# Kernel tuning notes

Hardware: AMD Instinct MI355X
Metric: run time of the kernel (lower is better)

Reference implementation:

```python
import jax, jax.numpy as jnp
import numpy as np

SM_STEPS = 10

def setup_inputs() -> dict:
    key = jax.random.key(0)
    k0, k1, k2, k3 = jax.random.split(key, 4)
    B, N, D, A = 8, 2048, 512, 128
    X = jax.random.normal(k0, (B, N, D), jnp.float32)
    adj = jax.random.uniform(k1, (B, N, N), jnp.float32)
    adj = adj / jnp.sum(adj, axis=-1, keepdims=True)  # row-stochastic for stable diffusion
    mask = jnp.ones((B, N), jnp.float32)
    W1 = jax.random.normal(k2, (A, D), jnp.float32) / np.sqrt(D).astype(np.float32)
    b1 = jnp.zeros((A,), jnp.float32)
    w2 = jax.random.normal(k3, (1, A), jnp.float32) / np.sqrt(A).astype(np.float32)
    alpha_logit = jnp.zeros((), jnp.float32)  # trainable alpha = sigmoid(0) = 0.5
    return {"X": X, "adj": adj, "mask": mask, "W1": W1, "b1": b1, "w2": w2, "alpha_logit": alpha_logit}

def _sm(f, adj, alpha, num_steps):
    # approx Sm: g <- alpha * adj @ g + (1 - alpha) * f, iterated num_steps times
    def body(g, _):
        g = alpha * jnp.einsum('bij,bjd->bid', adj, g) + (1.0 - alpha) * f
        return g, None
    g, _ = jax.lax.scan(body, f, None, length=num_steps)
    return g

def reference(X, adj, mask, W1, b1, w2, alpha_logit):
    alpha = jax.nn.sigmoid(alpha_logit)
    Xs = _sm(X, adj, alpha, SM_STEPS)                     # sm_where == 'early'
    H = jnp.einsum('bnd,ad->bna', Xs, W1) + b1            # proj1: (B,N,att_dim)
    H = jax.nn.gelu(H, approximate=False)                 # torch gelu (erf)
    f = jnp.einsum('bna,oa->bno', H, w2)                  # proj2: (B,N,1)
    m = mask[..., None]                                   # (B,N,1)
    logits = jnp.where(m > 0, f, -jnp.inf)
    s = jax.nn.softmax(logits, axis=1)                    # masked softmax over bag dim
    z = jnp.einsum('bnd,bno->bd', Xs, s)                  # bmm(X^T, s).squeeze(-1)
    return z
```

## Files before the change

### kernel.cpp

```cpp
#include <hip/hip_runtime.h>

constexpr int BB = 8;
constexpr int NN = 2048;
constexpr int DD = 512;
constexpr int AA = 128;
constexpr int SM_STEPS = 10;

typedef __attribute__((ext_vector_type(8))) short bf16x8;
typedef __attribute__((ext_vector_type(4))) float f32x4;
typedef __attribute__((ext_vector_type(8))) unsigned short u16x8;

__device__ __forceinline__ float bf2f(unsigned short u) {
  unsigned int v = ((unsigned int)u) << 16;
  union { unsigned int i; float f; } c; c.i = v; return c.f;
}
__device__ __forceinline__ unsigned short f2bf(float f) {
  union { float f; unsigned int i; } c; c.f = f;
  unsigned int v = c.i;
  unsigned int r = (v + 0x7FFFu + ((v >> 16) & 1u)) >> 16;
  return (unsigned short)r;
}

#define GLOBAL_AS __attribute__((address_space(1)))
#define LDS_AS __attribute__((address_space(3)))

__device__ __forceinline__ void async16(const void* g, void* l) {
  __builtin_amdgcn_global_load_lds((GLOBAL_AS const void*)g, (LDS_AS void*)l, 16, 0, 0);
}

__global__ __launch_bounds__(256) void convert_adj_kernel(
    const float* __restrict__ adj, unsigned short* __restrict__ adjb) {
  size_t i = (size_t)blockIdx.x * blockDim.x + threadIdx.x;
  size_t total = (size_t)BB * NN * NN / 4;
  size_t stride = (size_t)gridDim.x * blockDim.x;
  for (; i < total; i += stride) {
    float4 v = ((const float4*)adj)[i];
    ushort4 o;
    o.x = f2bf(v.x); o.y = f2bf(v.y); o.z = f2bf(v.z); o.w = f2bf(v.w);
    ((ushort4*)adjb)[i] = o;
  }
}

__global__ __launch_bounds__(256) void convert_w1_kernel(
    const float* __restrict__ W1, unsigned short* __restrict__ w1b) {
  int i = blockIdx.x * 256 + threadIdx.x;
  float4 v = ((const float4*)W1)[i];
  ushort4 o;
  o.x = f2bf(v.x); o.y = f2bf(v.y); o.z = f2bf(v.z); o.w = f2bf(v.w);
  ((ushort4*)w1b)[i] = o;
}

__global__ __launch_bounds__(256) void transpose_x_kernel(
    const float* __restrict__ X, unsigned short* __restrict__ xt) {
  __shared__ float tile[64][65];
  const int b = blockIdx.z;
  const int n0 = blockIdx.x * 64, d0 = blockIdx.y * 64;
  const int t = threadIdx.x;
  for (int i = 0; i < 16; ++i) {
    int idx = t + i * 256;
    int r = idx >> 6, c = idx & 63;
    tile[r][c] = X[(size_t)b * NN * DD + (size_t)(n0 + r) * DD + d0 + c];
  }
  __syncthreads();
  for (int i = 0; i < 16; ++i) {
    int idx = t + i * 256;
    int r = idx >> 6, c = idx & 63;
    xt[(size_t)b * DD * NN + (size_t)(d0 + r) * NN + n0 + c] = f2bf(tile[c][r]);
  }
}

__global__ __launch_bounds__(256) void transpose_xs_kernel(
    const unsigned short* __restrict__ xst, unsigned short* __restrict__ gnorm) {
  __shared__ unsigned int tile[64][65];
  const int b = blockIdx.z;
  const int n0 = blockIdx.x * 64, d0 = blockIdx.y * 64;
  const int t = threadIdx.x;
  for (int i = 0; i < 16; ++i) {
    int idx = t + i * 256;
    int r = idx >> 6, c = idx & 63;
    tile[r][c] = xst[(size_t)b * DD * NN + (size_t)(d0 + r) * NN + n0 + c];
  }
  __syncthreads();
  for (int i = 0; i < 16; ++i) {
    int idx = t + i * 256;
    int r = idx >> 6, c = idx & 63;
    gnorm[(size_t)b * NN * DD + (size_t)(n0 + r) * DD + d0 + c] =
        (unsigned short)tile[c][r];
  }
}

__global__ __launch_bounds__(512) void sm_step_kernel(
    const unsigned short* __restrict__ adjb,
    const unsigned short* __restrict__ gin,
    const unsigned short* __restrict__ xt,
    unsigned short* __restrict__ gout,
    const float* __restrict__ alogit) {
  constexpr int BK = 64;
  __shared__ alignas(16) unsigned char Abuf[3][128 * BK * 2];
  __shared__ alignas(16) unsigned char Bbuf[3][256 * BK * 2];

  const int t = threadIdx.x;
  const int b = blockIdx.z;
  const int m0 = blockIdx.y * 128;
  const int n0 = blockIdx.x * 256;

  const int lane = t & 63;
  const int wave = t >> 6;
  const int wr = wave >> 2;
  const int wc = wave & 3;
  const int ln = lane & 15, kq = lane >> 4;

  const unsigned short* gA = gin + (size_t)b * DD * NN;
  const unsigned short* gB = adjb + (size_t)b * NN * NN;
  const unsigned short* aSrc[2];
  const unsigned short* bSrc[4];
  int aOff[2], bOff[4];
#pragma unroll
  for (int u = 0; u < 2; ++u) {
    int o = u * 8192 + t * 16;
    int q = o ^ (((o >> 7) & 7) << 4);
    int row = q >> 7, colb = q & 127;
    aSrc[u] = gA + (size_t)(m0 + row) * NN + colb / 2;
    aOff[u] = o;
  }
#pragma unroll
  for (int u = 0; u < 4; ++u) {
    int o = u * 8192 + t * 16;
    int q = o ^ (((o >> 7) & 7) << 4);
    int row = q >> 7, colb = q & 127;
    bSrc[u] = gB + (size_t)(n0 + row) * NN + colb / 2;
    bOff[u] = o;
  }

  f32x4 acc[4][4];
#pragma unroll
  for (int i = 0; i < 4; ++i)
#pragma unroll
    for (int j = 0; j < 4; ++j) acc[i][j] = {0.f, 0.f, 0.f, 0.f};

  auto phase = [&](const unsigned char* Ab, const unsigned char* Bb, int ss,
                   int stg, int tnext) {
    bf16x8 av[4], bv[4];
#pragma unroll
    for (int ii = 0; ii < 4; ++ii) {
      int row = wr * 64 + ii * 16 + ln;
      int o = (row * 128 + ss * 64 + kq * 16) ^ ((row & 7) << 4);
      av[ii] = *(const bf16x8*)(Ab + o);
    }
#pragma unroll
    for (int jj = 0; jj < 4; ++jj) {
      int row = wc * 64 + jj * 16 + ln;
      int o = (row * 128 + ss * 64 + kq * 16) ^ ((row & 7) << 4);
      bv[jj] = *(const bf16x8*)(Bb + o);
    }
    if (stg == 1) {
      const int sl = tnext % 3;
      async16(aSrc[0] + tnext * BK, &Abuf[sl][aOff[0]]);
      async16(aSrc[1] + tnext * BK, &Abuf[sl][aOff[1]]);
      async16(bSrc[0] + tnext * BK, &Bbuf[sl][bOff[0]]);
    } else if (stg == 2) {
      const int sl = tnext % 3;
      async16(bSrc[1] + tnext * BK, &Bbuf[sl][bOff[1]]);
      async16(bSrc[2] + tnext * BK, &Bbuf[sl][bOff[2]]);
      async16(bSrc[3] + tnext * BK, &Bbuf[sl][bOff[3]]);
    }
    __builtin_amdgcn_s_barrier();
    asm volatile("s_waitcnt lgkmcnt(0)" ::: "memory");
    __builtin_amdgcn_sched_barrier(0);
    __builtin_amdgcn_s_setprio(1);
#pragma unroll
    for (int ii = 0; ii < 4; ++ii)
#pragma unroll
      for (int jj = 0; jj < 4; ++jj)
        acc[ii][jj] = __builtin_amdgcn_mfma_f32_16x16x32_bf16(av[ii], bv[jj],
                                                              acc[ii][jj], 0, 0, 0);
    __builtin_amdgcn_s_setprio(0);
    __builtin_amdgcn_s_barrier();
  };

#pragma unroll
  for (int tv = 0; tv < 2; ++tv) {
    const int sl = tv;
    async16(aSrc[0] + tv * BK, &Abuf[sl][aOff[0]]);
    async16(aSrc[1] + tv * BK, &Abuf[sl][aOff[1]]);
    async16(bSrc[0] + tv * BK, &Bbuf[sl][bOff[0]]);
    async16(bSrc[1] + tv * BK, &Bbuf[sl][bOff[1]]);
    async16(bSrc[2] + tv * BK, &Bbuf[sl][bOff[2]]);
    async16(bSrc[3] + tv * BK, &Bbuf[sl][bOff[3]]);
  }

  for (int tk = 0; tk < 30; ++tk) {
    const int sl = tk % 3;
    const unsigned char* Ab = Abuf[sl];
    const unsigned char* Bb = Bbuf[sl];
    asm volatile("s_waitcnt vmcnt(6)" ::: "memory");
    __builtin_amdgcn_s_barrier();
    phase(Ab, Bb, 0, 1, tk + 2);
    phase(Ab, Bb, 1, 2, tk + 2);
  }
  asm volatile("s_waitcnt vmcnt(6)" ::: "memory");
  __builtin_amdgcn_s_barrier();
  phase(Abuf[0], Bbuf[0], 0, 0, 0);
  phase(Abuf[0], Bbuf[0], 1, 0, 0);
  asm volatile("s_waitcnt vmcnt(0)" ::: "memory");
  __builtin_amdgcn_s_barrier();
  phase(Abuf[1], Bbuf[1], 0, 0, 0);
  phase(Abuf[1], Bbuf[1], 1, 0, 0);

  const float al = alogit[0];
  const float alpha = 1.0f / (1.0f + expf(-al));
  const float ia = 1.0f - alpha;

#pragma unroll
  for (int i = 0; i < 4; ++i) {
#pragma unroll
    for (int j = 0; j < 4; ++j) {
      const int mbase = m0 + wr * 64 + i * 16 + kq * 4;
      const int nn = n0 + wc * 64 + j * 16 + ln;
#pragma unroll
      for (int r = 0; r < 4; ++r) {
        size_t idx = (size_t)b * DD * NN + (size_t)(mbase + r) * NN + nn;
        float xv = bf2f(xt[idx]);
        gout[idx] = f2bf(alpha * acc[i][j][r] + ia * xv);
      }
    }
  }
}

__global__ __launch_bounds__(256) void proj_gemm_kernel(
    const unsigned short* __restrict__ gnorm,
    const unsigned short* __restrict__ w1b,
    const float* __restrict__ b1,
    const float* __restrict__ w2,
    float* __restrict__ fbuf) {
  constexpr int BK = 64;
  __shared__ alignas(16) unsigned short As[128 * BK];
  __shared__ alignas(16) unsigned short Bs[128 * BK];
  __shared__ float red[4][64];

  const int t = threadIdx.x;
  const int b = blockIdx.y;
  const int n0 = blockIdx.x * 128;

  const int lane = t & 63;
  const int wave = t >> 6;
  const int wr = wave >> 1, wc = wave & 1;
  const int ln = lane & 15, kq = lane >> 4;

  const unsigned short* gA =
      gnorm + (size_t)b * NN * DD + (size_t)(n0 + (t >> 3)) * DD + (t & 7) * 8;
  const unsigned short* gB = w1b + (size_t)(t >> 3) * DD + (t & 7) * 8;

  f32x4 acc[4][4];
#pragma unroll
  for (int i = 0; i < 4; ++i)
#pragma unroll
    for (int j = 0; j < 4; ++j) acc[i][j] = {0.f, 0.f, 0.f, 0.f};

  for (int k0 = 0; k0 < DD; k0 += BK) {
#pragma unroll
    for (int c = 0; c < 4; ++c) {
      async16(gA + (size_t)(32 * c) * DD, As + 8 * t + 2048 * c);
      async16(gB + (size_t)(32 * c) * DD, Bs + 8 * t + 2048 * c);
    }
    gA += BK;
    gB += BK;
    asm volatile("s_waitcnt vmcnt(0)" ::: "memory");
    __syncthreads();

#pragma unroll
    for (int s = 0; s < 2; ++s) {
      bf16x8 af[4], bfr[4];
#pragma unroll
      for (int i = 0; i < 4; ++i)
        af[i] = *(const bf16x8*)(&As[(wr * 64 + i * 16 + ln) * BK + s * 32 + kq * 8]);
#pragma unroll
      for (int j = 0; j < 4; ++j)
        bfr[j] = *(const bf16x8*)(&Bs[(wc * 64 + j * 16 + ln) * BK + s * 32 + kq * 8]);
#pragma unroll
      for (int i = 0; i < 4; ++i)
#pragma unroll
        for (int j = 0; j < 4; ++j)
          acc[i][j] =
              __builtin_amdgcn_mfma_f32_16x16x32_bf16(af[i], bfr[j], acc[i][j], 0, 0, 0);
    }
    __syncthreads();
  }

  float b1v[4], w2v[4];
#pragma unroll
  for (int j = 0; j < 4; ++j) {
    int a = wc * 64 + j * 16 + ln;
    b1v[j] = b1[a];
    w2v[j] = w2[a];
  }
  float p[4][4];
#pragma unroll
  for (int i = 0; i < 4; ++i)
#pragma unroll
    for (int r = 0; r < 4; ++r) {
      float s = 0.f;
#pragma unroll
      for (int j = 0; j < 4; ++j) {
        float x = acc[i][j][r] + b1v[j];
        float g = 0.5f * x * (1.0f + erff(x * 0.70710678118654752f));
        s += g * w2v[j];
      }
      p[i][r] = s;
    }
#pragma unroll
  for (int m = 1; m < 16; m <<= 1)
#pragma unroll
    for (int i = 0; i < 4; ++i)
#pragma unroll
      for (int r = 0; r < 4; ++r) p[i][r] += __shfl_xor(p[i][r], m);

  if (ln == 0) {
#pragma unroll
    for (int i = 0; i < 4; ++i)
#pragma unroll
      for (int r = 0; r < 4; ++r) red[wave][i * 16 + kq * 4 + r] = p[i][r];
  }
  __syncthreads();
  if (t < 128) {
    int w0 = (t >> 6) * 2, loc = t & 63;
    fbuf[(size_t)b * NN + n0 + t] = red[w0][loc] + red[w0 + 1][loc];
  }
}

__global__ __launch_bounds__(256) void softmax_kernel(
    const float* __restrict__ fbuf, const float* __restrict__ mask,
    float* __restrict__ sbuf) {
  __shared__ float red[8];
  const int b = blockIdx.x, t = threadIdx.x;
  float v[8];
  float mx = -INFINITY;
  for (int i = 0; i < 8; ++i) {
    int n = t + i * 256;
    float mk = mask[(size_t)b * NN + n];
    float lv = fbuf[(size_t)b * NN + n];
    v[i] = (mk > 0.f) ? lv : -INFINITY;
    mx = fmaxf(mx, v[i]);
  }
  for (int d = 32; d; d >>= 1) mx = fmaxf(mx, __shfl_xor(mx, d));
  if ((t & 63) == 0) red[t >> 6] = mx;
  __syncthreads();
  mx = fmaxf(fmaxf(red[0], red[1]), fmaxf(red[2], red[3]));
  float sum = 0.f;
  float e[8];
  for (int i = 0; i < 8; ++i) {
    e[i] = (v[i] == -INFINITY) ? 0.f : expf(v[i] - mx);
    sum += e[i];
  }
  for (int d = 32; d; d >>= 1) sum += __shfl_xor(sum, d);
  if ((t & 63) == 0) red[4 + (t >> 6)] = sum;
  __syncthreads();
  sum = red[4] + red[5] + red[6] + red[7];
  float inv = 1.0f / sum;
  for (int i = 0; i < 8; ++i) sbuf[(size_t)b * NN + t + i * 256] = e[i] * inv;
}

__global__ __launch_bounds__(256) void pool_kernel(
    const unsigned short* __restrict__ xst, const float* __restrict__ sbuf,
    float* __restrict__ zout) {
  __shared__ float sL[NN];
  const int b = blockIdx.y, t = threadIdx.x;
  const int d0 = blockIdx.x * 8;
  for (int i = 0; i < 8; ++i) sL[t + i * 256] = sbuf[(size_t)b * NN + t + i * 256];
  __syncthreads();
  const int row = t >> 5, c = t & 31;
  const int d = d0 + row;
  const unsigned short* xr = xst + (size_t)b * DD * NN + (size_t)d * NN;
  float acc = 0.f;
  for (int i = 0; i < 8; ++i) {
    int nb = c * 64 + i * 8;
    u16x8 x = *(const u16x8*)(xr + nb);
#pragma unroll
    for (int j = 0; j < 8; ++j) acc += bf2f((unsigned short)x[j]) * sL[nb + j];
  }
  for (int dlt = 16; dlt; dlt >>= 1) acc += __shfl_xor(acc, dlt);
  if (c == 0) zout[(size_t)b * DD + d] = acc;
}

extern "C" void kernel_launch(void* const* d_in, const int* in_sizes, int n_in,
                              void* d_out, int out_size, void* d_ws, size_t ws_size,
                              hipStream_t stream) {
  const float* X = (const float*)d_in[0];
  const float* adj = (const float*)d_in[1];
  const float* mask = (const float*)d_in[2];
  const float* W1 = (const float*)d_in[3];
  const float* b1 = (const float*)d_in[4];
  const float* w2 = (const float*)d_in[5];
  const float* alogit = (const float*)d_in[6];
  float* zout = (float*)d_out;

  char* ws = (char*)d_ws;
  unsigned short* adjb = (unsigned short*)ws;
  unsigned short* w1b = (unsigned short*)ws;
  unsigned short* xt = (unsigned short*)(ws + ((size_t)64 << 20));
  unsigned short* gnorm = (unsigned short*)(ws + ((size_t)64 << 20));
  unsigned short* p0 = (unsigned short*)(ws + ((size_t)80 << 20));
  unsigned short* p1 = (unsigned short*)(ws + ((size_t)96 << 20));
  float* fbuf = (float*)(ws + ((size_t)112 << 20));
  float* sbuf = (float*)(ws + ((size_t)112 << 20) + 65536);

  hipLaunchKernelGGL(convert_adj_kernel, dim3(2048), dim3(256), 0, stream, adj, adjb);
  hipLaunchKernelGGL(transpose_x_kernel, dim3(32, 8, 8), dim3(256), 0, stream, X, xt);

  const unsigned short* gin = xt;
  unsigned short* pp[2] = {p0, p1};
  for (int s = 0; s < SM_STEPS; ++s) {
    unsigned short* go = pp[s & 1];
    hipLaunchKernelGGL(sm_step_kernel, dim3(8, 4, 8), dim3(512), 0, stream, adjb, gin,
                       xt, go, alogit);
    gin = go;
  }

  hipLaunchKernelGGL(convert_w1_kernel, dim3(64), dim3(256), 0, stream, W1, w1b);
  hipLaunchKernelGGL(transpose_xs_kernel, dim3(32, 8, 8), dim3(256), 0, stream, gin,
                     gnorm);
  hipLaunchKernelGGL(proj_gemm_kernel, dim3(16, 8), dim3(256), 0, stream, gnorm, w1b,
                     b1, w2, fbuf);
  hipLaunchKernelGGL(softmax_kernel, dim3(8), dim3(256), 0, stream, fbuf, mask, sbuf);
  hipLaunchKernelGGL(pool_kernel, dim3(64, 8), dim3(256), 0, stream, gin, sbuf, zout);
}
```

Baseline: 486.5 us.

## Collapse two-phase barrier-heavy K-loop into single-barrier full-tile compute

Replaces the per-tile two half-phase scheme with one step per K tile. Each step has a single barrier at the top, issues all six async global-to-LDS copies for the tile two ahead, then reads both K halves from LDS and runs all 32 MFMAs. This removes three of the four workgroup barriers and the explicit lgkmcnt waits per tile, cutting synchronisation stalls. In exchange it drops the deliberate interleaving of LDS reads, copies and MFMA bursts across waves, and it holds twice as many operand registers live.

```diff
diff --git a/kernel.cpp b/kernel.cpp
--- a/kernel.cpp
+++ b/kernel.cpp
@@ -138,45 +138,28 @@
 #pragma unroll
     for (int j = 0; j < 4; ++j) acc[i][j] = {0.f, 0.f, 0.f, 0.f};
 
-  auto phase = [&](const unsigned char* Ab, const unsigned char* Bb, int ss,
-                   int stg, int tnext) {
-    bf16x8 av[4], bv[4];
-#pragma unroll
-    for (int ii = 0; ii < 4; ++ii) {
-      int row = wr * 64 + ii * 16 + ln;
-      int o = (row * 128 + ss * 64 + kq * 16) ^ ((row & 7) << 4);
-      av[ii] = *(const bf16x8*)(Ab + o);
-    }
-#pragma unroll
-    for (int jj = 0; jj < 4; ++jj) {
-      int row = wc * 64 + jj * 16 + ln;
-      int o = (row * 128 + ss * 64 + kq * 16) ^ ((row & 7) << 4);
-      bv[jj] = *(const bf16x8*)(Bb + o);
-    }
-    if (stg == 1) {
-      const int sl = tnext % 3;
-      async16(aSrc[0] + tnext * BK, &Abuf[sl][aOff[0]]);
-      async16(aSrc[1] + tnext * BK, &Abuf[sl][aOff[1]]);
-      async16(bSrc[0] + tnext * BK, &Bbuf[sl][bOff[0]]);
-    } else if (stg == 2) {
-      const int sl = tnext % 3;
-      async16(bSrc[1] + tnext * BK, &Bbuf[sl][bOff[1]]);
-      async16(bSrc[2] + tnext * BK, &Bbuf[sl][bOff[2]]);
-      async16(bSrc[3] + tnext * BK, &Bbuf[sl][bOff[3]]);
-    }
-    __builtin_amdgcn_s_barrier();
-    asm volatile("s_waitcnt lgkmcnt(0)" ::: "memory");
-    __builtin_amdgcn_sched_barrier(0);
-    __builtin_amdgcn_s_setprio(1);
-#pragma unroll
-    for (int ii = 0; ii < 4; ++ii)
-#pragma unroll
-      for (int jj = 0; jj < 4; ++jj)
-        acc[ii][jj] = __builtin_amdgcn_mfma_f32_16x16x32_bf16(av[ii], bv[jj],
-                                                              acc[ii][jj], 0, 0, 0);
-    __builtin_amdgcn_s_setprio(0);
-    __builtin_amdgcn_s_barrier();
-  };
+#define AOFF(ii, ss) \
+  (((wr * 64 + (ii)*16 + ln) * 128 + (ss)*64 + kq * 16) ^ (((wr * 64 + (ii)*16 + ln) & 7) << 4))
+#define BOFF(jj, ss) \
+  (((wc * 64 + (jj)*16 + ln) * 128 + (ss)*64 + kq * 16) ^ (((wc * 64 + (jj)*16 + ln) & 7) << 4))
+
+#define COMPUTE_TILE(Ab_, Bb_)                                                 \
+  do {                                                                         \
+    bf16x8 av[4][2], bv[4][2];                                                 \
+    _Pragma("unroll") for (int ii = 0; ii < 4; ++ii)                           \
+        _Pragma("unroll") for (int ss = 0; ss < 2; ++ss)                       \
+            av[ii][ss] = *(const bf16x8*)((Ab_) + AOFF(ii, ss));               \
+    _Pragma("unroll") for (int jj = 0; jj < 4; ++jj)                           \
+        _Pragma("unroll") for (int ss = 0; ss < 2; ++ss)                       \
+            bv[jj][ss] = *(const bf16x8*)((Bb_) + BOFF(jj, ss));               \
+    __builtin_amdgcn_s_setprio(1);                                             \
+    _Pragma("unroll") for (int ii = 0; ii < 4; ++ii)                           \
+        _Pragma("unroll") for (int jj = 0; jj < 4; ++jj)                       \
+            _Pragma("unroll") for (int ss = 0; ss < 2; ++ss)                   \
+                acc[ii][jj] = __builtin_amdgcn_mfma_f32_16x16x32_bf16(         \
+                    av[ii][ss], bv[jj][ss], acc[ii][jj], 0, 0, 0);             \
+    __builtin_amdgcn_s_setprio(0);                                             \
+  } while (0)
 
 #pragma unroll
   for (int tv = 0; tv < 2; ++tv) {
@@ -191,21 +174,28 @@
 
   for (int tk = 0; tk < 30; ++tk) {
     const int sl = tk % 3;
-    const unsigned char* Ab = Abuf[sl];
-    const unsigned char* Bb = Bbuf[sl];
+    const int sn = (tk + 2) % 3;
+    const int kk = (tk + 2) * BK;
     asm volatile("s_waitcnt vmcnt(6)" ::: "memory");
     __builtin_amdgcn_s_barrier();
-    phase(Ab, Bb, 0, 1, tk + 2);
-    phase(Ab, Bb, 1, 2, tk + 2);
+    async16(aSrc[0] + kk, &Abuf[sn][aOff[0]]);
+    async16(aSrc[1] + kk, &Abuf[sn][aOff[1]]);
+    async16(bSrc[0] + kk, &Bbuf[sn][bOff[0]]);
+    async16(bSrc[1] + kk, &Bbuf[sn][bOff[1]]);
+    async16(bSrc[2] + kk, &Bbuf[sn][bOff[2]]);
+    async16(bSrc[3] + kk, &Bbuf[sn][bOff[3]]);
+    COMPUTE_TILE(Abuf[sl], Bbuf[sl]);
   }
   asm volatile("s_waitcnt vmcnt(6)" ::: "memory");
   __builtin_amdgcn_s_barrier();
-  phase(Abuf[0], Bbuf[0], 0, 0, 0);
-  phase(Abuf[0], Bbuf[0], 1, 0, 0);
+  COMPUTE_TILE(Abuf[0], Bbuf[0]);
   asm volatile("s_waitcnt vmcnt(0)" ::: "memory");
   __builtin_amdgcn_s_barrier();
-  phase(Abuf[1], Bbuf[1], 0, 0, 0);
-  phase(Abuf[1], Bbuf[1], 1, 0, 0);
+  COMPUTE_TILE(Abuf[1], Bbuf[1]);
+
+#undef COMPUTE_TILE
+#undef AOFF
+#undef BOFF
 
   const float al = alogit[0];
   const float alpha = 1.0f / (1.0f + expf(-al));
```

After: 555.6 us. +14.2%, slower.
